# Performance work log

Hardware: AMD Instinct MI355X
Metric: run time of the kernel (lower is better)

## Reference

```python
import jax, jax.numpy as jnp
import numpy as np

SCALE = 10.0
DIM = 512
DIM_HEAD = 64
HEADS = DIM // DIM_HEAD
LN_EPS = 1e-05
L2_EPS = 1e-12


def l2norm(t, axis=1):
    # Faithful to source: default axis=1 (token axis for [b, n, h, d] tensors)
    denom = jnp.clip(jnp.linalg.norm(t, ord=2, axis=axis, keepdims=True), L2_EPS)
    return t / denom


def setup_inputs() -> dict:
    key = jax.random.key(0)
    k1, k2, k3 = jax.random.split(key, 3)
    B, H, W, C = 8, 32, 32, 512
    x = jax.random.normal(k1, (B, H, W, C), dtype=jnp.float32)
    ln_scale = jnp.ones((C,), dtype=jnp.float32)
    # 1x1 convs == channel matmuls; fan-in scaled init
    w_qkv = jax.random.normal(k2, (C, 3 * DIM), dtype=jnp.float32) / np.sqrt(C)
    w_out = jax.random.normal(k3, (DIM, C), dtype=jnp.float32) / np.sqrt(DIM)
    b_out = jnp.zeros((C,), dtype=jnp.float32)
    return {"x": x, "ln_scale": ln_scale, "w_qkv": w_qkv, "w_out": w_out, "b_out": b_out}


def reference(x, ln_scale, w_qkv, w_out, b_out):
    B, H, W, C = x.shape
    N = H * W
    # LayerNorm over channels (use_bias=False, use_scale=True)
    mean = jnp.mean(x, axis=-1, keepdims=True)
    var = jnp.mean(jnp.square(x - mean), axis=-1, keepdims=True)
    y = (x - mean) * jax.lax.rsqrt(var + LN_EPS) * ln_scale
    # 1x1 conv QKV projection (no bias)
    qkv = jnp.einsum('bhwc,cf->bhwf', y, w_qkv)  # [B,H,W,3*DIM]
    q, k, v = jnp.split(qkv, 3, axis=-1)
    # b x y (h d) -> b (x y) h d
    def to_tokens(t):
        return t.reshape(B, N, HEADS, DIM_HEAD)
    q, k, v = map(to_tokens, (q, k, v))
    # l2norm over axis=1 (token axis), faithful to source default
    q = l2norm(q)
    k = l2norm(k)
    sim = jnp.einsum('bihd,bjhd->bhij', q, k) * SCALE  # [B,heads,N,N]
    attn = jax.nn.softmax(sim, axis=-1)
    out = jnp.einsum('bhij,bjhd->bhid', attn, v)  # [B,heads,N,d]
    # b h (x y) d -> b x y (h d)
    out = out.transpose(0, 2, 1, 3).reshape(B, H, W, HEADS * DIM_HEAD)
    # 1x1 output conv (with bias)
    out = jnp.einsum('bhwf,fc->bhwc', out, w_out) + b_out
    return out
```

## Files before the change

### kernel.cpp

```cpp
#include <hip/hip_runtime.h>

typedef __bf16 bf16x8 __attribute__((ext_vector_type(8)));
typedef float f32x4 __attribute__((ext_vector_type(4)));
typedef float f32x16 __attribute__((ext_vector_type(16)));

#define DEV static __device__ __forceinline__

DEV unsigned short f2bf(float f) {
    union { __bf16 h; unsigned short s; } c; c.h = (__bf16)f; return c.s;
}
DEV float bf2f(unsigned short h) {
    union { unsigned u; float f; } c; c.u = ((unsigned)h) << 16; return c.f;
}
DEV unsigned packbf2(float a, float b) {
    union { __bf16 h[2]; unsigned u; } c;
    c.h[0] = (__bf16)a; c.h[1] = (__bf16)b; return c.u;
}

DEV f32x4 mfma16(bf16x8 a, bf16x8 b, f32x4 c) {
    return __builtin_amdgcn_mfma_f32_16x16x32_bf16(a, b, c, 0, 0, 0);
}
DEV f32x16 mfma32(bf16x8 a, bf16x8 b, f32x16 c) {
    return __builtin_amdgcn_mfma_f32_32x32x16_bf16(a, b, c, 0, 0, 0);
}

#define GLOAD16(gp, lp)                                                        \
    __builtin_amdgcn_global_load_lds(                                          \
        (const __attribute__((address_space(1))) unsigned int*)(gp),           \
        (__attribute__((address_space(3))) unsigned int*)(lp), 16, 0, 0)

__global__ __launch_bounds__(256) void ln_conv_kernel(const float* __restrict__ x,
                                                      const float* __restrict__ lnsc,
                                                      unsigned short* __restrict__ y,
                                                      float* __restrict__ ssq,
                                                      const float* __restrict__ wqkv,
                                                      const float* __restrict__ wout,
                                                      unsigned short* __restrict__ wqkvt,
                                                      unsigned short* __restrict__ woutt) {
    const int t = threadIdx.x;
    if (blockIdx.x >= 2048) {
        __shared__ __bf16 tile[64][65];
        const int wblk = blockIdx.x - 2048;
        const float* src;
        unsigned short* dst;
        int ldsrc, k0, f0;
        if (wblk < 192) {
            src = wqkv; dst = wqkvt; ldsrc = 1536;
            k0 = (wblk / 24) * 64; f0 = (wblk % 24) * 64;
        } else {
            int w2 = wblk - 192;
            src = wout; dst = woutt; ldsrc = 512;
            k0 = (w2 >> 3) * 64; f0 = (w2 & 7) * 64;
        }
#pragma unroll
        for (int j = 0; j < 16; j++) {
            int idx = t + j * 256;
            int a = idx >> 6, b2 = idx & 63;
            tile[b2][a] = (__bf16)src[(size_t)(k0 + a) * ldsrc + f0 + b2];
        }
        __syncthreads();
#pragma unroll
        for (int j = 0; j < 16; j++) {
            int idx = t + j * 256;
            int fb = idx >> 6, kc = idx & 63;
            union { __bf16 h; unsigned short s; } cv;
            cv.h = tile[fb][kc];
            dst[(size_t)(f0 + fb) * 512 + k0 + kc] = cv.s;
        }
        return;
    }
    if (blockIdx.x < 32) ssq[(blockIdx.x << 8) | t] = 0.0f;
    const int token = blockIdx.x * 4 + (t >> 6);
    const int lane = t & 63;
    const float4* xp = (const float4*)(x + (size_t)token * 512 + lane * 8);
    float4 v0 = xp[0], v1 = xp[1];
    float s = v0.x + v0.y + v0.z + v0.w + v1.x + v1.y + v1.z + v1.w;
    float s2 = v0.x * v0.x + v0.y * v0.y + v0.z * v0.z + v0.w * v0.w +
               v1.x * v1.x + v1.y * v1.y + v1.z * v1.z + v1.w * v1.w;
#pragma unroll
    for (int off = 1; off < 64; off <<= 1) {
        s += __shfl_xor(s, off);
        s2 += __shfl_xor(s2, off);
    }
    const float mean = s * (1.0f / 512.0f);
    const float var = s2 * (1.0f / 512.0f) - mean * mean;
    const float rstd = rsqrtf(var + 1e-5f);
    const float4* sp = (const float4*)(lnsc + lane * 8);
    float4 sc0 = sp[0], sc1 = sp[1];
    union { __bf16 h[8]; uint4 v; } pk;
    pk.h[0] = (__bf16)((v0.x - mean) * rstd * sc0.x);
    pk.h[1] = (__bf16)((v0.y - mean) * rstd * sc0.y);
    pk.h[2] = (__bf16)((v0.z - mean) * rstd * sc0.z);
    pk.h[3] = (__bf16)((v0.w - mean) * rstd * sc0.w);
    pk.h[4] = (__bf16)((v1.x - mean) * rstd * sc1.x);
    pk.h[5] = (__bf16)((v1.y - mean) * rstd * sc1.y);
    pk.h[6] = (__bf16)((v1.z - mean) * rstd * sc1.z);
    pk.h[7] = (__bf16)((v1.w - mean) * rstd * sc1.w);
    *(uint4*)(y + (size_t)token * 512 + lane * 8) = pk.v;
}

template <int WM, int WN, int NCOLS, bool OUT_BF16, bool BIAS, bool QKV, bool DB>
__global__ __launch_bounds__(256) void gemm_bt(const unsigned short* __restrict__ A,
                                               const unsigned short* __restrict__ Bt,
                                               void* __restrict__ Cout,
                                               const float* __restrict__ bias,
                                               float* __restrict__ ssq,
                                               unsigned short* __restrict__ kst,
                                               unsigned short* __restrict__ vst,
                                               int M, int K) {
    constexpr int BM = 2 * WM, BN = 2 * WN;
    constexpr int ASZ = BM * 64 * 2, BSZ = BN * 64 * 2;
    constexpr int NLA = WM / 16, NLB = WN / 16;
    constexpr int NBUF = DB ? 2 : 1;
    constexpr int STG = NBUF * (ASZ + BSZ);
    constexpr int TTB = QKV ? 128 * 136 * 2 : 0;
    constexpr int LDSB = STG > TTB ? STG : TTB;
    __shared__ __align__(16) char smem[LDSB];
    const int t = threadIdx.x;
    const int w = t >> 6, lane = t & 63;
    const int g = lane >> 4, l15 = lane & 15;
    const int wr = w >> 1, wc = w & 1;
    const int bR = blockIdx.x, bC = blockIdx.y;
    f32x4 acc[NLA][NLB] = {};
    const size_t ldb = (size_t)K * 2;
    const char* Ag = (const char*)A + (size_t)bR * BM * ldb;
    const char* Bg = (const char*)Bt + (size_t)bC * BN * ldb;

#define GSTAGE(buf, kt_)                                                            \
    {                                                                               \
        char* Ad = smem + (buf) * (ASZ + BSZ);                                      \
        char* Bd = Ad + ASZ;                                                        \
        _Pragma("unroll") for (int i = 0; i < NLA; i++) {                           \
            int o = i * 4096 + t * 16;                                              \
            int row = o >> 7, kb = (o & 127) ^ ((row & 7) << 4);                    \
            GLOAD16(Ag + (size_t)row * ldb + (size_t)(kt_) * 2 + kb, Ad + o);       \
        }                                                                           \
        _Pragma("unroll") for (int i = 0; i < NLB; i++) {                           \
            int o = i * 4096 + t * 16;                                              \
            int row = o >> 7, kb = (o & 127) ^ ((row & 7) << 4);                    \
            GLOAD16(Bg + (size_t)row * ldb + (size_t)(kt_) * 2 + kb, Bd + o);       \
        }                                                                           \
    }

#define GCOMPUTE(buf)                                                               \
    {                                                                               \
        const char* Ab = smem + (buf) * (ASZ + BSZ);                                \
        const char* Bb = Ab + ASZ;                                                  \
        _Pragma("unroll") for (int kk = 0; kk < 64; kk += 32) {                     \
            bf16x8 a[NLA], bb[NLB];                                                 \
            _Pragma("unroll") for (int m = 0; m < NLA; m++) {                       \
                int row = wr * WM + m * 16 + l15;                                   \
                int kb = ((kk + g * 8) * 2) ^ ((row & 7) << 4);                     \
                a[m] = *(const bf16x8*)(Ab + row * 128 + kb);                       \
            }                                                                       \
            _Pragma("unroll") for (int n = 0; n < NLB; n++) {                       \
                int row = wc * WN + n * 16 + l15;                                   \
                int kb = ((kk + g * 8) * 2) ^ ((row & 7) << 4);                     \
                bb[n] = *(const bf16x8*)(Bb + row * 128 + kb);                      \
            }                                                                       \
            _Pragma("unroll") for (int m = 0; m < NLA; m++)                         \
                _Pragma("unroll") for (int n = 0; n < NLB; n++)                     \
                    acc[m][n] = mfma16(a[m], bb[n], acc[m][n]);                     \
        }                                                                           \
    }

    const int NT = K >> 6;
    if constexpr (DB) {
        GSTAGE(0, 0)
        for (int tt = 0; tt < NT; ++tt) {
            const int cur = tt & 1;
            if (tt + 1 < NT) {
                GSTAGE(cur ^ 1, (tt + 1) * 64)
                asm volatile("s_waitcnt vmcnt(%0)" ::"n"(NLA + NLB) : "memory");
            } else {
                asm volatile("s_waitcnt vmcnt(0)" ::: "memory");
            }
            __builtin_amdgcn_s_barrier();
            GCOMPUTE(cur)
            __builtin_amdgcn_s_barrier();
        }
    } else {
        for (int tt = 0; tt < NT; ++tt) {
            __syncthreads();
            GSTAGE(0, tt * 64)
            asm volatile("s_waitcnt vmcnt(0)" ::: "memory");
            __syncthreads();
            GCOMPUTE(0)
        }
    }
#undef GSTAGE
#undef GCOMPUTE

    const int rbase = bR * BM + wr * WM;
    const int cbase = bC * BN + wc * WN;
    if (!QKV || bC < 4) {
#pragma unroll
        for (int m = 0; m < NLA; m++)
#pragma unroll
            for (int n = 0; n < NLB; n++)
#pragma unroll
                for (int r = 0; r < 4; r++) {
                    int row = rbase + m * 16 + g * 4 + r;
                    int col = cbase + n * 16 + l15;
                    float v = acc[m][n][r];
                    if constexpr (OUT_BF16)
                        ((unsigned short*)Cout)[(size_t)row * NCOLS + col] = f2bf(v);
                    else
                        ((float*)Cout)[(size_t)row * NCOLS + col] =
                            v + (BIAS ? bias[col] : 0.f);
                }
    }
    if constexpr (QKV) {
        if (bC < 8) {
            const int bb2 = bR >> 3;
#pragma unroll
            for (int n = 0; n < NLB; n++) {
                float ps = 0.f;
#pragma unroll
                for (int m = 0; m < NLA; m++)
#pragma unroll
                    for (int r = 0; r < 4; r++) ps += acc[m][n][r] * acc[m][n][r];
                ps += __shfl_xor(ps, 16);
                ps += __shfl_xor(ps, 32);
                if (g == 0)
                    atomicAdd(&ssq[bb2 * 1024 + cbase + n * 16 + l15], ps);
            }
        }
        if (bC >= 4) {
            unsigned short* TT = (unsigned short*)smem;
            const bool isK = bC < 8;
            __syncthreads();
#pragma unroll
            for (int m = 0; m < NLA; m++)
#pragma unroll
                for (int n = 0; n < NLB; n++)
#pragma unroll
                    for (int r = 0; r < 4; r++) {
                        int row = wr * WM + m * 16 + g * 4 + r;
                        int col = wc * WN + n * 16 + l15;
                        if (isK)
                            TT[row * 136 + col] = f2bf(acc[m][n][r]);
                        else
                            TT[col * 136 + row] = f2bf(acc[m][n][r]);
                    }
            __syncthreads();
            const int b2 = bR >> 3, rb = bR & 7;
            if (isK) {
#pragma unroll
                for (int j = 0; j < 8; j++) {
                    int sl = (t >> 7) + j * 2;
                    int nl = t & 127;
                    int hh = (bC - 4) * 2 + (sl >> 3), s = sl & 7;
                    *(uint4*)(kst +
                              (((size_t)(b2 * 8 + hh) * 8 + s) * 1024 + rb * 128 + nl) *
                                  8) = *(const uint4*)(TT + nl * 136 + sl * 8);
                }
            } else {
#pragma unroll
                for (int j = 0; j < 8; j++) {
                    int fl = t & 127;
                    int svl = (t >> 7) + j * 2;
                    int hh = (bC - 8) * 2 + (fl >> 6), d = fl & 63;
                    *(uint4*)(vst +
                              (((size_t)(b2 * 8 + hh) * 128 + rb * 16 + svl) * 64 + d) *
                                  8) = *(const uint4*)(TT + fl * 136 + svl * 8);
                }
            }
        }
    }
}

__global__ __launch_bounds__(256) void attn_kernel(const unsigned short* __restrict__ qbuf,
                                                   const unsigned short* __restrict__ kst,
                                                   const unsigned short* __restrict__ vst,
                                                   unsigned short* __restrict__ attnout,
                                                   const float* __restrict__ ssq) {
    __shared__ unsigned short Ks[2][4096];
    __shared__ unsigned short Vs[2][4096];
    __shared__ float smq[64];
    const int t = threadIdx.x, w = t >> 6, lane = t & 63;
    const int hi = lane >> 5, q31 = lane & 31;
    const int qt = blockIdx.y, bh = blockIdx.x;
    const int b = bh >> 3, h = bh & 7;
    const size_t qrow0 = (size_t)b * 1024 + qt * 128;
    const char* kstb = (const char*)kst + (size_t)bh * 131072;
    const char* vstb = (const char*)vst + (size_t)bh * 131072;

    if (t < 64) {
        float nq = fmaxf(sqrtf(ssq[b * 1024 + h * 64 + t]), 1e-12f);
        float nk = fmaxf(sqrtf(ssq[b * 1024 + 512 + h * 64 + t]), 1e-12f);
        smq[t] = 14.42695040888963f / (nq * nk);
    }
    __syncthreads();

    bf16x8 qf[4];
#pragma unroll
    for (int ds = 0; ds < 4; ds++) {
        union { bf16x8 v; unsigned short u[8]; } in, ov;
        in.v = *(const bf16x8*)(qbuf + (qrow0 + w * 32 + q31) * 512 + h * 64 +
                                ds * 16 + hi * 8);
#pragma unroll
        for (int j = 0; j < 8; j++)
            ov.u[j] = f2bf(bf2f(in.u[j]) * smq[ds * 16 + hi * 8 + j]);
        qf[ds] = ov.v;
    }

    f32x16 accO[2] = {};
    float prs = 0.f;

#define ASTAGE(buf, tt_)                                                            \
    {                                                                               \
        _Pragma("unroll") for (int i = 0; i < 2; i++) {                             \
            const int s = i * 4 + w;                                                \
            const int o = i * 4096 + t * 16;                                        \
            GLOAD16(kstb + (((size_t)s * 1024 + (tt_) * 64 + lane) << 4),           \
                    (char*)Ks[buf] + o);                                            \
            GLOAD16(vstb + (((size_t)(tt_) * 512 + s * 64 + lane) << 4),            \
                    (char*)Vs[buf] + o);                                            \
        }                                                                           \
    }

    ASTAGE(0, 0)
    for (int tt = 0; tt < 16; ++tt) {
        const int cur = tt & 1;
        if (tt < 15) {
            ASTAGE(cur ^ 1, tt + 1)
            asm volatile("s_waitcnt vmcnt(4)" ::: "memory");
        } else {
            asm volatile("s_waitcnt vmcnt(0)" ::: "memory");
        }
        __builtin_amdgcn_s_barrier();

#pragma unroll
        for (int kvb = 0; kvb < 2; kvb++) {
            f32x16 sa = {};
            __builtin_amdgcn_s_setprio(1);
#pragma unroll
            for (int ds = 0; ds < 4; ds++) {
                bf16x8 kf = *(const bf16x8*)((const char*)Ks[cur] +
                                             ((ds * 2 + hi) << 10) +
                                             ((kvb * 32 + q31) << 4));
                sa = mfma32(kf, qf[ds], sa);
            }
            __builtin_amdgcn_s_setprio(0);
            float p[16];
#pragma unroll
            for (int r = 0; r < 16; r++) {
                p[r] = __builtin_amdgcn_exp2f(sa[r]);
                prs += p[r];
            }
            bf16x8 pf[2];
#pragma unroll
            for (int s2 = 0; s2 < 2; s2++) {
                unsigned a0 = packbf2(p[s2 * 8 + 0], p[s2 * 8 + 1]);
                unsigned a1 = packbf2(p[s2 * 8 + 2], p[s2 * 8 + 3]);
                unsigned b0 = packbf2(p[s2 * 8 + 4], p[s2 * 8 + 5]);
                unsigned b1 = packbf2(p[s2 * 8 + 6], p[s2 * 8 + 7]);
                asm volatile("v_permlane32_swap_b32 %0, %1" : "+v"(a0), "+v"(b0));
                asm volatile("v_permlane32_swap_b32 %0, %1" : "+v"(a1), "+v"(b1));
                union { unsigned u[4]; bf16x8 v; } fr;
                fr.u[0] = a0; fr.u[1] = a1; fr.u[2] = b0; fr.u[3] = b1;
                pf[s2] = fr.v;
            }
            __builtin_amdgcn_s_setprio(1);
#pragma unroll
            for (int s2 = 0; s2 < 2; s2++)
#pragma unroll
                for (int dvb = 0; dvb < 2; dvb++) {
                    bf16x8 vf = *(const bf16x8*)((const char*)Vs[cur] +
                                                 ((kvb * 4 + s2 * 2 + hi) << 10) +
                                                 ((dvb * 32 + q31) << 4));
                    accO[dvb] = mfma32(vf, pf[s2], accO[dvb]);
                }
            __builtin_amdgcn_s_setprio(0);
        }
        __builtin_amdgcn_s_barrier();
    }
#undef ASTAGE

    const float tot = prs + __shfl_xor(prs, 32);
    const float inv = 1.0f / tot;
    unsigned short* orow = attnout + (qrow0 + w * 32 + q31) * 512 + h * 64;
#pragma unroll
    for (int dvb = 0; dvb < 2; dvb++)
#pragma unroll
        for (int grp = 0; grp < 4; grp++) {
            float f0 = accO[dvb][grp * 4 + 0] * inv;
            float f1 = accO[dvb][grp * 4 + 1] * inv;
            float f2 = accO[dvb][grp * 4 + 2] * inv;
            float f3 = accO[dvb][grp * 4 + 3] * inv;
            uint2 pk;
            pk.x = packbf2(f0, f1);
            pk.y = packbf2(f2, f3);
            *(uint2*)(orow + dvb * 32 + grp * 8 + 4 * hi) = pk;
        }
}

extern "C" void kernel_launch(void* const* d_in, const int* in_sizes, int n_in,
                              void* d_out, int out_size, void* d_ws, size_t ws_size,
                              hipStream_t stream) {
    const float* x = (const float*)d_in[0];
    const float* ln_scale = (const float*)d_in[1];
    const float* w_qkv = (const float*)d_in[2];
    const float* w_out = (const float*)d_in[3];
    const float* b_out = (const float*)d_in[4];
    float* out = (float*)d_out;

    char* ws = (char*)d_ws;
    unsigned short* y = (unsigned short*)(ws + 0);
    unsigned short* wqkvt = (unsigned short*)(ws + 8388608);
    unsigned short* woutt = (unsigned short*)(ws + 9961472);
    unsigned short* qbuf = (unsigned short*)(ws + 10485760);
    unsigned short* kst = (unsigned short*)(ws + 18874368);
    unsigned short* vst = (unsigned short*)(ws + 27262976);
    float* ssq = (float*)(ws + 35651584);
    unsigned short* attnout = (unsigned short*)(ws + 0);

    ln_conv_kernel<<<2304, 256, 0, stream>>>(x, ln_scale, y, ssq, w_qkv, w_out, wqkvt,
                                             woutt);
    gemm_bt<64, 64, 512, true, false, true, false>
        <<<dim3(64, 12), 256, 0, stream>>>(y, wqkvt, qbuf, nullptr, ssq, kst, vst,
                                           8192, 512);
    attn_kernel<<<dim3(64, 8), 256, 0, stream>>>(qbuf, kst, vst, attnout, ssq);
    gemm_bt<32, 64, 512, false, true, false, true>
        <<<dim3(128, 4), 256, 0, stream>>>(attnout, woutt, out, b_out, nullptr, nullptr,
                                           nullptr, 8192, 512);
}
```

Measured before the change: 71.40 us.

## Load K/V fragments directly from global into registers, drop LDS staging

The attention kernel no longer stages K and V tiles through double-buffered shared memory with async global-to-LDS loads and block barriers. Each wave now loads its own MFMA fragments straight from global memory into registers, ping-ponging two register sets so the next 32-key step's loads are issued before the current step's compute. This removes LDS traffic and the two barriers per tile. In exchange, the four waves each fetch the same K/V data separately (more global/L2 traffic), the loop is fully unrolled, and register pressure rises.

```diff
diff --git a/kernel.cpp b/kernel.cpp
--- a/kernel.cpp
+++ b/kernel.cpp
@@ -275,8 +275,6 @@
                                                    const unsigned short* __restrict__ vst,
                                                    unsigned short* __restrict__ attnout,
                                                    const float* __restrict__ ssq) {
-    __shared__ unsigned short Ks[2][4096];
-    __shared__ unsigned short Vs[2][4096];
     __shared__ float smq[64];
     const int t = threadIdx.x, w = t >> 6, lane = t & 63;
     const int hi = lane >> 5, q31 = lane & 31;
@@ -308,75 +306,70 @@
     f32x16 accO[2] = {};
     float prs = 0.f;
 
-#define ASTAGE(buf, tt_)                                                            \
+#define LOADK(dst, s_)                                                              \
     {                                                                               \
-        _Pragma("unroll") for (int i = 0; i < 2; i++) {                             \
-            const int s = i * 4 + w;                                                \
-            const int o = i * 4096 + t * 16;                                        \
-            GLOAD16(kstb + (((size_t)s * 1024 + (tt_) * 64 + lane) << 4),           \
-                    (char*)Ks[buf] + o);                                            \
-            GLOAD16(vstb + (((size_t)(tt_) * 512 + s * 64 + lane) << 4),            \
-                    (char*)Vs[buf] + o);                                            \
+        const int tt_ = (s_) >> 1, kvb_ = (s_)&1;                                   \
+        _Pragma("unroll") for (int ds = 0; ds < 4; ds++)                            \
+            dst[ds] = *(const bf16x8*)(kstb +                                       \
+                ((size_t)((ds * 2 + hi) * 1024 + tt_ * 64 + kvb_ * 32 + q31) << 4)); \
+    }
+#define LOADV(dst, s_)                                                              \
+    {                                                                               \
+        const int tt_ = (s_) >> 1, kvb_ = (s_)&1;                                   \
+        _Pragma("unroll") for (int s2 = 0; s2 < 2; s2++)                            \
+            _Pragma("unroll") for (int dvb = 0; dvb < 2; dvb++)                     \
+                dst[s2 * 2 + dvb] = *(const bf16x8*)(vstb +                         \
+                    ((size_t)(tt_ * 512 + (kvb_ * 4 + s2 * 2 + hi) * 64 +           \
+                              dvb * 32 + q31) << 4));                               \
+    }
+#define ACOMPUTE(kf, vf)                                                            \
+    {                                                                               \
+        f32x16 sa = {};                                                             \
+        __builtin_amdgcn_s_setprio(1);                                              \
+        _Pragma("unroll") for (int ds = 0; ds < 4; ds++)                            \
+            sa = mfma32(kf[ds], qf[ds], sa);                                        \
+        __builtin_amdgcn_s_setprio(0);                                              \
+        float p[16];                                                                \
+        _Pragma("unroll") for (int r = 0; r < 16; r++) {                            \
+            p[r] = __builtin_amdgcn_exp2f(sa[r]);                                   \
+            prs += p[r];                                                            \
         }                                                                           \
-    }
-
-    ASTAGE(0, 0)
-    for (int tt = 0; tt < 16; ++tt) {
-        const int cur = tt & 1;
-        if (tt < 15) {
-            ASTAGE(cur ^ 1, tt + 1)
-            asm volatile("s_waitcnt vmcnt(4)" ::: "memory");
-        } else {
-            asm volatile("s_waitcnt vmcnt(0)" ::: "memory");
-        }
-        __builtin_amdgcn_s_barrier();
-
-#pragma unroll
-        for (int kvb = 0; kvb < 2; kvb++) {
-            f32x16 sa = {};
-            __builtin_amdgcn_s_setprio(1);
-#pragma unroll
-            for (int ds = 0; ds < 4; ds++) {
-                bf16x8 kf = *(const bf16x8*)((const char*)Ks[cur] +
-                                             ((ds * 2 + hi) << 10) +
-                                             ((kvb * 32 + q31) << 4));
-                sa = mfma32(kf, qf[ds], sa);
-            }
-            __builtin_amdgcn_s_setprio(0);
-            float p[16];
-#pragma unroll
-            for (int r = 0; r < 16; r++) {
-                p[r] = __builtin_amdgcn_exp2f(sa[r]);
-                prs += p[r];
-            }
-            bf16x8 pf[2];
-#pragma unroll
-            for (int s2 = 0; s2 < 2; s2++) {
-                unsigned a0 = packbf2(p[s2 * 8 + 0], p[s2 * 8 + 1]);
-                unsigned a1 = packbf2(p[s2 * 8 + 2], p[s2 * 8 + 3]);
-                unsigned b0 = packbf2(p[s2 * 8 + 4], p[s2 * 8 + 5]);
-                unsigned b1 = packbf2(p[s2 * 8 + 6], p[s2 * 8 + 7]);
-                asm volatile("v_permlane32_swap_b32 %0, %1" : "+v"(a0), "+v"(b0));
-                asm volatile("v_permlane32_swap_b32 %0, %1" : "+v"(a1), "+v"(b1));
-                union { unsigned u[4]; bf16x8 v; } fr;
-                fr.u[0] = a0; fr.u[1] = a1; fr.u[2] = b0; fr.u[3] = b1;
-                pf[s2] = fr.v;
-            }
-            __builtin_amdgcn_s_setprio(1);
-#pragma unroll
-            for (int s2 = 0; s2 < 2; s2++)
-#pragma unroll
-                for (int dvb = 0; dvb < 2; dvb++) {
-                    bf16x8 vf = *(const bf16x8*)((const char*)Vs[cur] +
-                                                 ((kvb * 4 + s2 * 2 + hi) << 10) +
-                                                 ((dvb * 32 + q31) << 4));
-                    accO[dvb] = mfma32(vf, pf[s2], accO[dvb]);
-                }
-            __builtin_amdgcn_s_setprio(0);
-        }
-        __builtin_amdgcn_s_barrier();
-    }
-#undef ASTAGE
+        bf16x8 pf[2];                                                               \
+        _Pragma("unroll") for (int s2 = 0; s2 < 2; s2++) {                          \
+            unsigned a0 = packbf2(p[s2 * 8 + 0], p[s2 * 8 + 1]);                    \
+            unsigned a1 = packbf2(p[s2 * 8 + 2], p[s2 * 8 + 3]);                    \
+            unsigned b0 = packbf2(p[s2 * 8 + 4], p[s2 * 8 + 5]);                    \
+            unsigned b1 = packbf2(p[s2 * 8 + 6], p[s2 * 8 + 7]);                    \
+            asm volatile("v_permlane32_swap_b32 %0, %1" : "+v"(a0), "+v"(b0));      \
+            asm volatile("v_permlane32_swap_b32 %0, %1" : "+v"(a1), "+v"(b1));      \
+            union { unsigned u[4]; bf16x8 v; } fr;                                  \
+            fr.u[0] = a0; fr.u[1] = a1; fr.u[2] = b0; fr.u[3] = b1;                 \
+            pf[s2] = fr.v;                                                          \
+        }                                                                           \
+        __builtin_amdgcn_s_setprio(1);                                              \
+        _Pragma("unroll") for (int s2 = 0; s2 < 2; s2++)                            \
+            _Pragma("unroll") for (int dvb = 0; dvb < 2; dvb++)                     \
+                accO[dvb] = mfma32(vf[s2 * 2 + dvb], pf[s2], accO[dvb]);            \
+        __builtin_amdgcn_s_setprio(0);                                              \
+    }
+
+    bf16x8 kA[4], vA[4], kB[4], vB[4];
+    LOADK(kA, 0)
+    LOADV(vA, 0)
+#pragma unroll
+    for (int s = 0; s < 32; s += 2) {
+        LOADK(kB, s + 1)
+        LOADV(vB, s + 1)
+        ACOMPUTE(kA, vA)
+        if (s + 2 < 32) {
+            LOADK(kA, s + 2)
+            LOADV(vA, s + 2)
+        }
+        ACOMPUTE(kB, vB)
+    }
+#undef LOADK
+#undef LOADV
+#undef ACOMPUTE
 
     const float tot = prs + __shfl_xor(prs, 32);
     const float inv = 1.0f / tot;
```

Result: slower. 128.4 us (+79.8%).

## Split attention KV range across two wave groups with LDS combine

Applied to the files above, without the earlier changes.

The attention kernel now runs 512 threads per block. Two groups of four waves each process half of the key/value sequence for the same 128 query rows, so the loop runs 8 iterations instead of 16. Partial output accumulators and row sums are then merged through shared memory before normalisation and store. Barriers in the GEMM and attention loops are also pinned with a scheduling barrier so the compiler cannot move code across them. The change is meant to add waves per CU and shorten the serial KV loop. In exchange it doubles LDS use to about 66KB per block and adds a final combine step.

```diff
diff --git a/kernel.cpp b/kernel.cpp
--- a/kernel.cpp
+++ b/kernel.cpp
@@ -28,6 +28,10 @@
     __builtin_amdgcn_global_load_lds(                                          \
         (const __attribute__((address_space(1))) unsigned int*)(gp),           \
         (__attribute__((address_space(3))) unsigned int*)(lp), 16, 0, 0)
+
+#define BARRIER_PINNED()                                                       \
+    __builtin_amdgcn_s_barrier();                                              \
+    __builtin_amdgcn_sched_barrier(0)
 
 __global__ __launch_bounds__(256) void ln_conv_kernel(const float* __restrict__ x,
                                                       const float* __restrict__ lnsc,
@@ -175,9 +179,9 @@
             } else {
                 asm volatile("s_waitcnt vmcnt(0)" ::: "memory");
             }
-            __builtin_amdgcn_s_barrier();
+            BARRIER_PINNED();
             GCOMPUTE(cur)
-            __builtin_amdgcn_s_barrier();
+            BARRIER_PINNED();
         }
     } else {
         for (int tt = 0; tt < NT; ++tt) {
@@ -270,16 +274,15 @@
     }
 }
 
-__global__ __launch_bounds__(256) void attn_kernel(const unsigned short* __restrict__ qbuf,
-                                                   const unsigned short* __restrict__ kst,
-                                                   const unsigned short* __restrict__ vst,
-                                                   unsigned short* __restrict__ attnout,
-                                                   const float* __restrict__ ssq) {
-    __shared__ unsigned short Ks[2][4096];
-    __shared__ unsigned short Vs[2][4096];
-    __shared__ float smq[64];
+__global__ __launch_bounds__(512, 4) void attn_kernel(
+    const unsigned short* __restrict__ qbuf, const unsigned short* __restrict__ kst,
+    const unsigned short* __restrict__ vst, unsigned short* __restrict__ attnout,
+    const float* __restrict__ ssq) {
+    __shared__ __align__(16) char smem[66048];
+    float* smq = (float*)(smem + 65536);
     const int t = threadIdx.x, w = t >> 6, lane = t & 63;
     const int hi = lane >> 5, q31 = lane & 31;
+    const int g2 = w >> 2, wq = w & 3;
     const int qt = blockIdx.y, bh = blockIdx.x;
     const int b = bh >> 3, h = bh & 7;
     const size_t qrow0 = (size_t)b * 1024 + qt * 128;
@@ -297,7 +300,7 @@
 #pragma unroll
     for (int ds = 0; ds < 4; ds++) {
         union { bf16x8 v; unsigned short u[8]; } in, ov;
-        in.v = *(const bf16x8*)(qbuf + (qrow0 + w * 32 + q31) * 512 + h * 64 +
+        in.v = *(const bf16x8*)(qbuf + (qrow0 + wq * 32 + q31) * 512 + h * 64 +
                                 ds * 16 + hi * 8);
 #pragma unroll
         for (int j = 0; j < 8; j++)
@@ -311,25 +314,27 @@
 #define ASTAGE(buf, tt_)                                                            \
     {                                                                               \
         _Pragma("unroll") for (int i = 0; i < 2; i++) {                             \
-            const int s = i * 4 + w;                                                \
-            const int o = i * 4096 + t * 16;                                        \
-            GLOAD16(kstb + (((size_t)s * 1024 + (tt_) * 64 + lane) << 4),           \
-                    (char*)Ks[buf] + o);                                            \
-            GLOAD16(vstb + (((size_t)(tt_) * 512 + s * 64 + lane) << 4),            \
-                    (char*)Vs[buf] + o);                                            \
+            const int c = i * 512 + t;                                              \
+            const int hk = c >> 9, sl = (c >> 6) & 7, tl = c & 63;                  \
+            GLOAD16(kstb + ((size_t)(sl * 1024 + hk * 512 + (tt_) * 64 + tl) << 4), \
+                    smem + (((buf)*2 + hk) << 13) + sl * 1024 + tl * 16);           \
+            GLOAD16(vstb + ((size_t)((hk * 64 + (tt_)*8 + sl) * 64 + tl) << 4),     \
+                    smem + 32768 + (((buf)*2 + hk) << 13) + sl * 1024 + tl * 16);   \
         }                                                                           \
     }
 
     ASTAGE(0, 0)
-    for (int tt = 0; tt < 16; ++tt) {
+    for (int tt = 0; tt < 8; ++tt) {
         const int cur = tt & 1;
-        if (tt < 15) {
+        if (tt < 7) {
             ASTAGE(cur ^ 1, tt + 1)
             asm volatile("s_waitcnt vmcnt(4)" ::: "memory");
         } else {
             asm volatile("s_waitcnt vmcnt(0)" ::: "memory");
         }
-        __builtin_amdgcn_s_barrier();
+        BARRIER_PINNED();
+        const char* KsH = smem + ((cur * 2 + g2) << 13);
+        const char* VsH = smem + 32768 + ((cur * 2 + g2) << 13);
 
 #pragma unroll
         for (int kvb = 0; kvb < 2; kvb++) {
@@ -337,8 +342,7 @@
             __builtin_amdgcn_s_setprio(1);
 #pragma unroll
             for (int ds = 0; ds < 4; ds++) {
-                bf16x8 kf = *(const bf16x8*)((const char*)Ks[cur] +
-                                             ((ds * 2 + hi) << 10) +
+                bf16x8 kf = *(const bf16x8*)(KsH + ((ds * 2 + hi) << 10) +
                                              ((kvb * 32 + q31) << 4));
                 sa = mfma32(kf, qf[ds], sa);
             }
@@ -367,33 +371,63 @@
             for (int s2 = 0; s2 < 2; s2++)
 #pragma unroll
                 for (int dvb = 0; dvb < 2; dvb++) {
-                    bf16x8 vf = *(const bf16x8*)((const char*)Vs[cur] +
-                                                 ((kvb * 4 + s2 * 2 + hi) << 10) +
+                    bf16x8 vf = *(const bf16x8*)(VsH + ((kvb * 4 + s2 * 2 + hi) << 10) +
                                                  ((dvb * 32 + q31) << 4));
                     accO[dvb] = mfma32(vf, pf[s2], accO[dvb]);
                 }
             __builtin_amdgcn_s_setprio(0);
         }
-        __builtin_amdgcn_s_barrier();
+        BARRIER_PINNED();
     }
 #undef ASTAGE
 
-    const float tot = prs + __shfl_xor(prs, 32);
-    const float inv = 1.0f / tot;
-    unsigned short* orow = attnout + (qrow0 + w * 32 + q31) * 512 + h * 64;
-#pragma unroll
-    for (int dvb = 0; dvb < 2; dvb++)
-#pragma unroll
-        for (int grp = 0; grp < 4; grp++) {
-            float f0 = accO[dvb][grp * 4 + 0] * inv;
-            float f1 = accO[dvb][grp * 4 + 1] * inv;
-            float f2 = accO[dvb][grp * 4 + 2] * inv;
-            float f3 = accO[dvb][grp * 4 + 3] * inv;
-            uint2 pk;
-            pk.x = packbf2(f0, f1);
-            pk.y = packbf2(f2, f3);
-            *(uint2*)(orow + dvb * 32 + grp * 8 + 4 * hi) = pk;
-        }
+    __syncthreads();
+    float* comb = (float*)smem;
+    float* pe = comb + (wq * 64 + lane) * 36;
+    if (g2 == 1) {
+        union { f32x16 v; float4 q[4]; } u0, u1;
+        u0.v = accO[0]; u1.v = accO[1];
+        *(float4*)(pe + 0) = u0.q[0];
+        *(float4*)(pe + 4) = u0.q[1];
+        *(float4*)(pe + 8) = u0.q[2];
+        *(float4*)(pe + 12) = u0.q[3];
+        *(float4*)(pe + 16) = u1.q[0];
+        *(float4*)(pe + 20) = u1.q[1];
+        *(float4*)(pe + 24) = u1.q[2];
+        *(float4*)(pe + 28) = u1.q[3];
+        pe[32] = prs;
+    }
+    __syncthreads();
+    if (g2 == 0) {
+        union { f32x16 v; float4 q[4]; } u0, u1;
+        u0.q[0] = *(const float4*)(pe + 0);
+        u0.q[1] = *(const float4*)(pe + 4);
+        u0.q[2] = *(const float4*)(pe + 8);
+        u0.q[3] = *(const float4*)(pe + 12);
+        u1.q[0] = *(const float4*)(pe + 16);
+        u1.q[1] = *(const float4*)(pe + 20);
+        u1.q[2] = *(const float4*)(pe + 24);
+        u1.q[3] = *(const float4*)(pe + 28);
+        accO[0] += u0.v;
+        accO[1] += u1.v;
+        prs += pe[32];
+        const float tot = prs + __shfl_xor(prs, 32);
+        const float inv = 1.0f / tot;
+        unsigned short* orow = attnout + (qrow0 + wq * 32 + q31) * 512 + h * 64;
+#pragma unroll
+        for (int dvb = 0; dvb < 2; dvb++)
+#pragma unroll
+            for (int grp = 0; grp < 4; grp++) {
+                float f0 = accO[dvb][grp * 4 + 0] * inv;
+                float f1 = accO[dvb][grp * 4 + 1] * inv;
+                float f2 = accO[dvb][grp * 4 + 2] * inv;
+                float f3 = accO[dvb][grp * 4 + 3] * inv;
+                uint2 pk;
+                pk.x = packbf2(f0, f1);
+                pk.y = packbf2(f2, f3);
+                *(uint2*)(orow + dvb * 32 + grp * 8 + 4 * hi) = pk;
+            }
+    }
 }
 
 extern "C" void kernel_launch(void* const* d_in, const int* in_sizes, int n_in,
@@ -421,7 +455,7 @@
     gemm_bt<64, 64, 512, true, false, true, false>
         <<<dim3(64, 12), 256, 0, stream>>>(y, wqkvt, qbuf, nullptr, ssq, kst, vst,
                                            8192, 512);
-    attn_kernel<<<dim3(64, 8), 256, 0, stream>>>(qbuf, kst, vst, attnout, ssq);
+    attn_kernel<<<dim3(64, 8), 512, 0, stream>>>(qbuf, kst, vst, attnout, ssq);
     gemm_bt<32, 64, 512, false, true, false, true>
         <<<dim3(128, 4), 256, 0, stream>>>(attnout, woutt, out, b_out, nullptr, nullptr,
                                            nullptr, 8192, 512);
```

Result: faster. 66.85 us (-6.4%).
